# Kernel optimization log

Measured on AMD Instinct MI355X. Metric: run time of the kernel, lower is better.

## Reference

```python
import jax, jax.numpy as jnp
import numpy as np

B = 4; E_PER = 100_000; E = B * E_PER
N_NODES = 50_000; N_REL = 500; D = 64; D_LG = 256
K_PER_VI = 20; S_VI = E // K_PER_VI          # 20000 sorted vi segments
S_VJ_PER = 5_000; S_VJ = B * S_VJ_PER        # 20000 unsorted vj segments
N_MEM = 131_072
INTERACT = ((0, 3), (0, 2, 3), (0, 4), (0, 2, 4), (1, 3), (1, 2, 3), (1, 4), (1, 2, 4))


def _build_edges():
    rng = np.random.default_rng(0)
    idx_vi = np.repeat(np.arange(S_VI), K_PER_VI)          # sorted segment ids
    gpb = S_VI // B
    eg = idx_vi // gpb                                     # sorted by eg_idx too
    vi = rng.integers(0, N_NODES, S_VI)[idx_vi]
    idx_vj = np.empty(E, dtype=np.int64)
    for b in range(B):
        loc = np.concatenate([np.arange(S_VJ_PER), rng.integers(0, S_VJ_PER, E_PER - S_VJ_PER)])
        rng.shuffle(loc)
        idx_vj[b * E_PER:(b + 1) * E_PER] = b * S_VJ_PER + loc  # every group non-empty
    vj = rng.integers(0, N_NODES, S_VJ)[idx_vj]            # consistent (eg, vj) per group
    rel = rng.integers(0, N_REL, E)
    e2vi = rng.integers(0, N_MEM, E)
    e2vj = rng.integers(0, N_MEM, E)
    return np.stack([eg, vi, vj, rel, idx_vi, idx_vj, e2vi, e2vj], axis=1).astype(np.int32)


def setup_inputs() -> dict:
    key = jax.random.key(0)
    ks = jax.random.split(key, 10)
    return {
        "node_attention": jax.random.uniform(ks[0], (B, N_NODES), jnp.float32),
        "scanned_edges": jnp.asarray(_build_edges()),
        "edges_y": jax.random.uniform(ks[1], (E,), jnp.float32),
        "hidden_uncon": jax.random.normal(ks[2], (1, N_NODES, D_LG), jnp.float32),
        "hidden_con": jax.random.normal(ks[3], (N_MEM, D), jnp.float32),
        "Wc": jax.random.normal(ks[4], (D, D), jnp.float32) / np.sqrt(D).astype(np.float32),
        "bc": jnp.zeros((D,), jnp.float32),
        "Wu": jax.random.normal(ks[5], (D_LG, D), jnp.float32) / np.sqrt(D_LG).astype(np.float32),
        "bu": jnp.zeros((D,), jnp.float32),
        "rel_table": jax.random.normal(ks[6], (N_REL, D), jnp.float32) * 0.05,
        "ws": jax.random.normal(ks[7], (len(INTERACT), D), jnp.float32) / np.sqrt(float(len(INTERACT))).astype(np.float32) if False else jax.random.normal(ks[7], (len(INTERACT), D), jnp.float32) * (1.0 / np.sqrt(len(INTERACT)).astype(np.float32)),
        "fb": jnp.zeros((D,), jnp.float32),
        "out_w": jax.random.normal(ks[8], (D,), jnp.float32),
        "out_b": jnp.zeros((D,), jnp.float32),
        "n_vi_segments": S_VI,
        "n_vj_segments": S_VJ,
    }


def reference(node_attention, scanned_edges, edges_y, hidden_uncon, hidden_con,
              Wc, bc, Wu, bu, rel_table, ws, fb, out_w, out_b,
              n_vi_segments, n_vj_segments):
    eg, vi, vj, rel = (scanned_edges[:, i] for i in range(4))
    idx_vi, idx_vj, e2vi, e2vj = (scanned_edges[:, i] for i in range(4, 8))
    # projections (proj_con / proj_uncon, tanh Dense)
    hc = jnp.tanh(hidden_con @ Wc + bc)          # [N_MEM, D]
    hu = jnp.tanh(hidden_uncon @ Wu + bu)[0]     # [n_nodes, D]; batch_size==1 path of Node2Edge
    # Node2Edge gathers
    feats = (hc[e2vi], hu[vi], rel_table[rel], hc[e2vj], hu[vj])  # each [E, D]
    # F layer: weighted sum of elementwise interaction products
    out = fb
    for k, idxs in enumerate(INTERACT):
        x = feats[idxs[0]]
        for i in idxs[1:]:
            x = x * feats[i]
        out = out + x * ws[k]
    out = jax.nn.relu(out) * out_w + out_b
    logits = jnp.sum(out, axis=1)                # [E]
    # NeighborSoftmax at 'vi' (sorted segment softmax)
    m = jax.ops.segment_max(logits, idx_vi, num_segments=n_vi_segments)
    ex = jnp.exp(logits - m[idx_vi])
    den = jax.ops.segment_sum(ex, idx_vi, num_segments=n_vi_segments)
    transition = ex / den[idx_vi]
    # attention flow: gather source attention, weight, aggregate at vj
    trans_att = transition * node_attention[eg, vi] * edges_y
    aggr = jax.ops.segment_sum(trans_att, idx_vj, num_segments=n_vj_segments)
    b_g = jax.ops.segment_max(eg, idx_vj, num_segments=n_vj_segments)
    vj_g = jax.ops.segment_max(vj, idx_vj, num_segments=n_vj_segments)
    new_node_attention = jnp.zeros_like(node_attention).at[b_g, vj_g].add(aggr)
    return new_node_attention
```

## Files before the change

kernel.cpp:

```cpp
#include <hip/hip_runtime.h>
#include <hip/hip_bf16.h>
#include <hip/hip_fp16.h>

#define D 64
#define KPER 20

typedef __attribute__((ext_vector_type(8))) short short8;
typedef __attribute__((ext_vector_type(4))) float floatx4;

__device__ __forceinline__ unsigned short f2bfu(float x) {
    __hip_bfloat16 h = __float2bfloat16(x);
    return *reinterpret_cast<unsigned short*>(&h);
}
__device__ __forceinline__ unsigned short f2hu(float x) {
    __half h = __float2half(x);
    return *reinterpret_cast<unsigned short*>(&h);
}
union UH2 { unsigned u; __half2 h; };
__device__ __forceinline__ __half2 u2h2(unsigned u) { UH2 x; x.u = u; return x.h; }

__device__ __forceinline__ unsigned cvt2bf(float lo, float hi) {
    unsigned r;
    asm("v_cvt_pk_bf16_f32 %0, %1, %2" : "=v"(r) : "v"(lo), "v"(hi));
    return r;
}

__device__ __forceinline__ __half2 pk_max(__half2 a, __half2 b) {
    __half2 r;
    asm("v_pk_max_f16 %0, %1, %2" : "=v"(r) : "v"(a), "v"(b));
    return r;
}

__device__ __forceinline__ float fast_tanh(float x) {
    float xc = fminf(fmaxf(x, -15.f), 15.f);
    float e = __expf(2.f * xc);
    return 1.f - 2.f * __builtin_amdgcn_rcpf(1.f + e);
}

template<int CTRL>
__device__ __forceinline__ float dpp_add(float x) {
    int t = __builtin_amdgcn_update_dpp(0, __float_as_int(x), CTRL, 0xf, 0xf, true);
    return x + __int_as_float(t);
}
template<int CTRL>
__device__ __forceinline__ float dpp_max(float x) {
    int xi = __float_as_int(x);
    int t = __builtin_amdgcn_update_dpp(xi, xi, CTRL, 0xf, 0xf, false);
    return fmaxf(x, __int_as_float(t));
}
__device__ __forceinline__ float wave_sum_b(float x) {
    x = dpp_add<0x111>(x); x = dpp_add<0x112>(x);
    x = dpp_add<0x114>(x); x = dpp_add<0x118>(x);
    x = dpp_add<0x142>(x); x = dpp_add<0x143>(x);
    return __int_as_float(__builtin_amdgcn_readlane(__float_as_int(x), 63));
}
__device__ __forceinline__ float wave_max_b(float x) {
    x = dpp_max<0x111>(x); x = dpp_max<0x112>(x);
    x = dpp_max<0x114>(x); x = dpp_max<0x118>(x);
    x = dpp_max<0x142>(x); x = dpp_max<0x143>(x);
    return __int_as_float(__builtin_amdgcn_readlane(__float_as_int(x), 63));
}
__device__ __forceinline__ float row16_sum(float x) {
    x = dpp_add<0x111>(x); x = dpp_add<0x112>(x);
    x = dpp_add<0x114>(x); x = dpp_add<0x118>(x);
    return x;
}

__global__ __launch_bounds__(256) void prep(
        const float* __restrict__ Wc, const float* __restrict__ Wu,
        const float* __restrict__ relf, const float* __restrict__ wsf,
        const float* __restrict__ fbf,
        unsigned short* __restrict__ Wcp, unsigned short* __restrict__ Wup,
        unsigned short* __restrict__ relb, unsigned short* __restrict__ wsh,
        unsigned short* __restrict__ fbh, float* __restrict__ outz,
        int nout, int nrel) {
    int tid = blockIdx.x * 256 + threadIdx.x;
    int nth = gridDim.x * 256;
    for (int i = tid; i < 4 * 2 * 64 * 8; i += nth) {
        int j = i & 7, lane = (i >> 3) & 63, f = i >> 9;
        int ct = f >> 1, kt = f & 1;
        int m = lane & 15, quad = lane >> 4;
        Wcp[i] = f2bfu(Wc[(kt * 32 + quad * 8 + j) * 64 + ct * 16 + m]);
    }
    for (int i = tid; i < 4 * 8 * 64 * 8; i += nth) {
        int j = i & 7, lane = (i >> 3) & 63, f = i >> 9;
        int ct = f >> 3, kt = f & 7;
        int m = lane & 15, quad = lane >> 4;
        Wup[i] = f2bfu(Wu[(kt * 32 + quad * 8 + j) * 64 + ct * 16 + m]);
    }
    for (int i = tid; i < nrel; i += nth) relb[i] = f2hu(relf[i]);
    for (int i = tid; i < 8 * D; i += nth) wsh[i] = f2hu(wsf[i]);
    for (int i = tid; i < D; i += nth) fbh[i] = f2hu(fbf[i]);
    for (int i = tid; i < nout; i += nth) outz[i] = 0.0f;
}

__device__ __forceinline__ void proj64_pair(const float* __restrict__ h,
        const unsigned short* __restrict__ Wp, const float* __restrict__ b,
        unsigned short* __restrict__ out, int rt0) {
    constexpr int K = 64, KT = 2, CTN = 4;
    int lane = threadIdx.x & 63;
    int m = lane & 15, quad = lane >> 4;
    short8 bfr[CTN][KT];
    #pragma unroll
    for (int ct = 0; ct < CTN; ++ct)
        #pragma unroll
        for (int kt = 0; kt < KT; ++kt)
            bfr[ct][kt] = *(const short8*)(Wp + (((ct * 2 + kt) * 64 + lane) << 3));
    float bv[CTN];
    #pragma unroll
    for (int ct = 0; ct < CTN; ++ct) bv[ct] = b[ct * 16 + m];
    int rt1 = rt0 + 1;
    const float* hrow0 = h + (size_t)(rt0 * 16 + m) * K + quad * 8;
    const float* hrow1 = h + (size_t)(rt1 * 16 + m) * K + quad * 8;
    floatx4 a0[KT][2], a1[KT][2];
    #pragma unroll
    for (int kt = 0; kt < KT; ++kt) {
        a0[kt][0] = *(const floatx4*)(hrow0 + kt * 32);
        a0[kt][1] = *(const floatx4*)(hrow0 + kt * 32 + 4);
        a1[kt][0] = *(const floatx4*)(hrow1 + kt * 32);
        a1[kt][1] = *(const floatx4*)(hrow1 + kt * 32 + 4);
    }
    #pragma unroll
    for (int t = 0; t < 2; ++t) {
        floatx4 (*ar)[2] = t ? a1 : a0;
        int rt = t ? rt1 : rt0;
        floatx4 acc[CTN];
        #pragma unroll
        for (int ct = 0; ct < CTN; ++ct) acc[ct] = floatx4{0.f, 0.f, 0.f, 0.f};
        #pragma unroll
        for (int kt = 0; kt < KT; ++kt) {
            union { uint4 u; short8 s; } cc;
            cc.u.x = cvt2bf(ar[kt][0][0], ar[kt][0][1]);
            cc.u.y = cvt2bf(ar[kt][0][2], ar[kt][0][3]);
            cc.u.z = cvt2bf(ar[kt][1][0], ar[kt][1][1]);
            cc.u.w = cvt2bf(ar[kt][1][2], ar[kt][1][3]);
            short8 af = cc.s;
            #pragma unroll
            for (int ct = 0; ct < CTN; ++ct)
                acc[ct] = __builtin_amdgcn_mfma_f32_16x16x32_bf16(af, bfr[ct][kt], acc[ct], 0, 0, 0);
        }
        #pragma unroll
        for (int ct = 0; ct < CTN; ++ct) {
            int col = ct * 16 + m;
            #pragma unroll
            for (int reg = 0; reg < 4; ++reg) {
                int row = rt * 16 + quad * 4 + reg;
                out[(size_t)row * 64 + col] = f2hu(fast_tanh(acc[ct][reg] + bv[ct]));
            }
        }
    }
}

__device__ __forceinline__ void proj256_body(const float* __restrict__ h,
        const unsigned short* __restrict__ Wp, const float* __restrict__ b,
        unsigned short* __restrict__ out, int ct0, int rt0, int rtstride, int ntiles) {
    constexpr int K = 256, KT = 8, CTN = 2;
    int lane = threadIdx.x & 63;
    int m = lane & 15, quad = lane >> 4;
    short8 bfr[CTN][KT];
    #pragma unroll
    for (int ct = 0; ct < CTN; ++ct)
        #pragma unroll
        for (int kt = 0; kt < KT; ++kt)
            bfr[ct][kt] = *(const short8*)(Wp + ((((ct0 + ct) * 8 + kt) * 64 + lane) << 3));
    float bv[CTN];
    #pragma unroll
    for (int ct = 0; ct < CTN; ++ct) bv[ct] = b[(ct0 + ct) * 16 + m];
    for (int rt = rt0; rt < ntiles; rt += rtstride) {
        floatx4 acc[CTN];
        #pragma unroll
        for (int ct = 0; ct < CTN; ++ct) acc[ct] = floatx4{0.f, 0.f, 0.f, 0.f};
        const float* hrow = h + (size_t)(rt * 16 + m) * K + quad * 8;
        #pragma unroll
        for (int kt = 0; kt < KT; ++kt) {
            floatx4 v0 = *(const floatx4*)(hrow + kt * 32);
            floatx4 v1 = *(const floatx4*)(hrow + kt * 32 + 4);
            union { uint4 u; short8 s; } cc;
            cc.u.x = cvt2bf(v0[0], v0[1]);
            cc.u.y = cvt2bf(v0[2], v0[3]);
            cc.u.z = cvt2bf(v1[0], v1[1]);
            cc.u.w = cvt2bf(v1[2], v1[3]);
            short8 af = cc.s;
            #pragma unroll
            for (int ct = 0; ct < CTN; ++ct)
                acc[ct] = __builtin_amdgcn_mfma_f32_16x16x32_bf16(af, bfr[ct][kt], acc[ct], 0, 0, 0);
        }
        #pragma unroll
        for (int ct = 0; ct < CTN; ++ct) {
            int col = (ct0 + ct) * 16 + m;
            #pragma unroll
            for (int reg = 0; reg < 4; ++reg) {
                int row = rt * 16 + quad * 4 + reg;
                out[(size_t)row * 64 + col] = f2hu(fast_tanh(acc[ct][reg] + bv[ct]));
            }
        }
    }
}

__global__ __launch_bounds__(256) void proj_fused(
        const float* __restrict__ hcon, const unsigned short* __restrict__ Wcp,
        const float* __restrict__ bc,
        const float* __restrict__ hun, const unsigned short* __restrict__ Wup,
        const float* __restrict__ bu,
        unsigned short* __restrict__ hc, unsigned short* __restrict__ hu,
        int t64, int t256, int g64, int g256) {
    int bid = blockIdx.x;
    int w = threadIdx.x >> 6;
    if (bid < g256) {
        int wid = bid * 4 + w;
        int half = wid & 1;
        proj256_body(hun, Wup, bu, hu, half * 2, wid >> 1, g256 * 2, t256);
    } else {
        int wid = (bid - g256) * 4 + w;
        proj64_pair(hcon, Wcp, bc, hc, wid * 2);
    }
}

__device__ __forceinline__ float edge_acc(
        uint2 G0, uint2 G2, uint2 G3, uint2 G4, uint2 F1u,
        const uint2* __restrict__ wku, uint2 fbu, floatx4 owv, __half2 z2) {
    float acc = 0.f;
    #pragma unroll
    for (int p = 0; p < 2; ++p) {
        __half2 F0 = u2h2(p ? G0.y : G0.x);
        __half2 F2 = u2h2(p ? G2.y : G2.x);
        __half2 F3 = u2h2(p ? G3.y : G3.x);
        __half2 F4 = u2h2(p ? G4.y : G4.x);
        __half2 f1 = u2h2(p ? F1u.y : F1u.x);
        __half2 fb2 = u2h2(p ? fbu.y : fbu.x);
        __half2 w0 = u2h2(p ? wku[0].y : wku[0].x);
        __half2 w1 = u2h2(p ? wku[1].y : wku[1].x);
        __half2 w2 = u2h2(p ? wku[2].y : wku[2].x);
        __half2 w3 = u2h2(p ? wku[3].y : wku[3].x);
        __half2 w4 = u2h2(p ? wku[4].y : wku[4].x);
        __half2 w5 = u2h2(p ? wku[5].y : wku[5].x);
        __half2 w6 = u2h2(p ? wku[6].y : wku[6].x);
        __half2 w7 = u2h2(p ? wku[7].y : wku[7].x);
        __half2 t1 = __hfma2(F2, w1, w0);
        __half2 t2 = __hfma2(F2, w5, w4);
        __half2 t3 = __hfma2(F2, w3, w2);
        __half2 t4 = __hfma2(F2, w7, w6);
        __half2 uu = __hfma2(F0, t1, __hmul2(f1, t2));
        __half2 vv = __hfma2(F0, t3, __hmul2(f1, t4));
        __half2 od = __hfma2(F3, uu, __hfma2(F4, vv, fb2));
        __half2 r  = pk_max(od, z2);
        float2 rf  = __half22float2(r);
        acc = fmaf(rf.x, owv[2 * p], fmaf(rf.y, owv[2 * p + 1], acc));
    }
    return acc;
}

__global__ __launch_bounds__(256) void edge_kernel(
        const float* __restrict__ natt, const int* __restrict__ edges,
        const float* __restrict__ ey, const unsigned short* __restrict__ hc,
        const unsigned short* __restrict__ hu, const unsigned short* __restrict__ relt,
        const unsigned short* __restrict__ wsh, const unsigned short* __restrict__ fbh,
        const float* __restrict__ outw, float* __restrict__ out, int N) {
    int lane = threadIdx.x & 63;
    int g = lane >> 4, sub = lane & 15;
    int l2 = lane >> 2;
    int wid = blockIdx.x * 4 + (threadIdx.x >> 6);
    long baseA = (long)(wid * 2) * KPER;
    long baseB = baseA + KPER;
    const int* ebA = edges + baseA * 8;
    const int* ebB = edges + baseB * 8;

    int2 h0A = *(const int2*)ebA;
    int2 h0B = *(const int2*)ebB;
    const int* egpA = ebA + g * 8;
    const int* egpB = ebB + g * 8;
    int2 m23A[5], m67A[5], m23B[5], m67B[5];
    #pragma unroll
    for (int i = 0; i < 5; ++i) {
        m23A[i] = *(const int2*)(egpA + i * 32 + 2);
        m67A[i] = *(const int2*)(egpA + i * 32 + 6);
        m23B[i] = *(const int2*)(egpB + i * 32 + 2);
        m67B[i] = *(const int2*)(egpB + i * 32 + 6);
    }
    int myvjA = 0, myvjB = 0; float eyA = 0.f, eyB = 0.f;
    if (lane < KPER) {
        myvjA = ebA[lane * 8 + 2];
        myvjB = ebB[lane * 8 + 2];
        eyA = ey[baseA + lane];
        eyB = ey[baseB + lane];
    }
    int egA = __builtin_amdgcn_readfirstlane(h0A.x);
    int viA = __builtin_amdgcn_readfirstlane(h0A.y);
    int egB = __builtin_amdgcn_readfirstlane(h0B.x);
    int viB = __builtin_amdgcn_readfirstlane(h0B.y);
    uint2 F1A = *(const uint2*)(hu + (size_t)viA * D + sub * 4);
    uint2 F1B = *(const uint2*)(hu + (size_t)viB * D + sub * 4);
    float naA = natt[(size_t)egA * N + viA];
    float naB = natt[(size_t)egB * N + viB];

    uint2 wku[8];
    #pragma unroll
    for (int k = 0; k < 8; ++k) wku[k] = *(const uint2*)(wsh + k * D + sub * 4);
    uint2 fbu = *(const uint2*)(fbh + sub * 4);
    floatx4 owv = *(const floatx4*)(outw + sub * 4);
    __half2 z2 = __float2half2_rn(0.f);

    float mylA = -INFINITY, mylB = -INFINITY;
    uint2 c0 = *(const uint2*)(hc   + (size_t)m67A[0].x * D + sub * 4);
    uint2 c2 = *(const uint2*)(relt + (size_t)m23A[0].y * D + sub * 4);
    uint2 c3 = *(const uint2*)(hc   + (size_t)m67A[0].y * D + sub * 4);
    uint2 c4 = *(const uint2*)(hu   + (size_t)m23A[0].x * D + sub * 4);
    #pragma unroll
    for (int t = 0; t < 10; ++t) {
        uint2 n0 = c0, n2 = c2, n3 = c3, n4 = c4;
        if (t < 9) {
            const int tn = t + 1;
            const int2* p23 = (tn < 5) ? m23A : m23B;
            const int2* p67 = (tn < 5) ? m67A : m67B;
            const int ii = (tn < 5) ? tn : tn - 5;
            n0 = *(const uint2*)(hc   + (size_t)p67[ii].x * D + sub * 4);
            n2 = *(const uint2*)(relt + (size_t)p23[ii].y * D + sub * 4);
            n3 = *(const uint2*)(hc   + (size_t)p67[ii].y * D + sub * 4);
            n4 = *(const uint2*)(hu   + (size_t)p23[ii].x * D + sub * 4);
        }
        __builtin_amdgcn_sched_barrier(0);
        uint2 F1 = (t < 5) ? F1A : F1B;
        float acc = edge_acc(c0, c2, c3, c4, F1, wku, fbu, owv, z2);
        float rs = row16_sum(acc);
        float tot = __shfl(rs, ((lane & 3) << 4) + 15);
        if (t < 5) mylA = (l2 == t) ? tot : mylA;
        else       mylB = (l2 == (t - 5)) ? tot : mylB;
        c0 = n0; c2 = n2; c3 = n3; c4 = n4;
    }

    float mxA = wave_max_b(mylA);
    float exA = __expf(mylA - mxA);
    float denA = wave_sum_b(exA);
    if (lane < KPER) {
        float t = (exA / denA) * naA * eyA;
        atomicAdd(out + (size_t)egA * N + myvjA, t);
    }
    float mxB = wave_max_b(mylB);
    float exB = __expf(mylB - mxB);
    float denB = wave_sum_b(exB);
    if (lane < KPER) {
        float t = (exB / denB) * naB * eyB;
        atomicAdd(out + (size_t)egB * N + myvjB, t);
    }
}

extern "C" void kernel_launch(void* const* d_in, const int* in_sizes, int n_in,
                              void* d_out, int out_size, void* d_ws, size_t ws_size,
                              hipStream_t stream) {
    const float* natt = (const float*)d_in[0];
    const int*   edges = (const int*)d_in[1];
    const float* ey   = (const float*)d_in[2];
    const float* hun  = (const float*)d_in[3];
    const float* hcon = (const float*)d_in[4];
    const float* Wc   = (const float*)d_in[5];
    const float* bc   = (const float*)d_in[6];
    const float* Wu   = (const float*)d_in[7];
    const float* bu   = (const float*)d_in[8];
    const float* relt = (const float*)d_in[9];
    const float* wsm  = (const float*)d_in[10];
    const float* fb   = (const float*)d_in[11];
    const float* outw = (const float*)d_in[12];
    float* out = (float*)d_out;

    int E    = in_sizes[2];
    int S    = E / KPER;
    int nmem = in_sizes[4] / D;
    int N    = in_sizes[3] / 256;
    int nrel = in_sizes[9];

    int t64  = nmem / 16;
    int t256 = N / 16;
    int g64  = t64 / 8;
    int g256 = 800;

    unsigned short* hc  = (unsigned short*)d_ws;
    unsigned short* hu  = hc + (size_t)nmem * D;
    unsigned short* rb  = hu + (size_t)N * D;
    unsigned short* Wcp = rb + nrel;
    unsigned short* Wup = Wcp + 4096;
    unsigned short* wsh = Wup + 16384;
    unsigned short* fbh = wsh + 8 * D;

    prep<<<64, 256, 0, stream>>>(Wc, Wu, relt, wsm, fb, Wcp, Wup, rb, wsh, fbh,
                                 out, out_size, nrel);
    proj_fused<<<g256 + g64, 256, 0, stream>>>(hcon, Wcp, bc, hun, Wup, bu,
                                               hc, hu, t64, t256, g64, g256);
    edge_kernel<<<S / 8, 256, 0, stream>>>(natt, edges, ey, hc, hu, rb,
                                           wsh, fbh, outw, out, N);
}
```

Before: 199.3 us.

## Gather 8 edges per wave with 16-byte loads and issue all gathers upfront

Remaps the edge kernel so each wave processes 8 edges at a time with 8 lanes per edge, using 16-byte vector loads instead of 8-byte ones. All gathers for both segments are issued before any compute, replacing the one-step software prefetch pipeline. The per-edge reduction shrinks to an 8-lane DPP sum. Register pressure rises sharply, which launch_bounds(256,3) tries to cap. The 20-edge segments also waste 4 of 24 edge slots per segment.

```diff
diff --git a/kernel.cpp b/kernel.cpp
--- a/kernel.cpp
+++ b/kernel.cpp
@@ -18,6 +18,9 @@
 }
 union UH2 { unsigned u; __half2 h; };
 __device__ __forceinline__ __half2 u2h2(unsigned u) { UH2 x; x.u = u; return x.h; }
+__device__ __forceinline__ unsigned pick4(uint4 v, int p) {
+    return p == 0 ? v.x : p == 1 ? v.y : p == 2 ? v.z : v.w;
+}
 
 __device__ __forceinline__ unsigned cvt2bf(float lo, float hi) {
     unsigned r;
@@ -60,9 +63,9 @@
     x = dpp_max<0x142>(x); x = dpp_max<0x143>(x);
     return __int_as_float(__builtin_amdgcn_readlane(__float_as_int(x), 63));
 }
-__device__ __forceinline__ float row16_sum(float x) {
+__device__ __forceinline__ float row8_sum(float x) {
     x = dpp_add<0x111>(x); x = dpp_add<0x112>(x);
-    x = dpp_add<0x114>(x); x = dpp_add<0x118>(x);
+    x = dpp_add<0x114>(x);
     return x;
 }
 
@@ -216,26 +219,27 @@
     }
 }
 
-__device__ __forceinline__ float edge_acc(
-        uint2 G0, uint2 G2, uint2 G3, uint2 G4, uint2 F1u,
-        const uint2* __restrict__ wku, uint2 fbu, floatx4 owv, __half2 z2) {
+__device__ __forceinline__ float edge_acc8(
+        uint4 G0, uint4 G2, uint4 G3, uint4 G4, uint4 F1,
+        const uint4* __restrict__ wk4, uint4 fb4,
+        floatx4 ow0, floatx4 ow1, __half2 z2) {
     float acc = 0.f;
     #pragma unroll
-    for (int p = 0; p < 2; ++p) {
-        __half2 F0 = u2h2(p ? G0.y : G0.x);
-        __half2 F2 = u2h2(p ? G2.y : G2.x);
-        __half2 F3 = u2h2(p ? G3.y : G3.x);
-        __half2 F4 = u2h2(p ? G4.y : G4.x);
-        __half2 f1 = u2h2(p ? F1u.y : F1u.x);
-        __half2 fb2 = u2h2(p ? fbu.y : fbu.x);
-        __half2 w0 = u2h2(p ? wku[0].y : wku[0].x);
-        __half2 w1 = u2h2(p ? wku[1].y : wku[1].x);
-        __half2 w2 = u2h2(p ? wku[2].y : wku[2].x);
-        __half2 w3 = u2h2(p ? wku[3].y : wku[3].x);
-        __half2 w4 = u2h2(p ? wku[4].y : wku[4].x);
-        __half2 w5 = u2h2(p ? wku[5].y : wku[5].x);
-        __half2 w6 = u2h2(p ? wku[6].y : wku[6].x);
-        __half2 w7 = u2h2(p ? wku[7].y : wku[7].x);
+    for (int p = 0; p < 4; ++p) {
+        __half2 F0 = u2h2(pick4(G0, p));
+        __half2 F2 = u2h2(pick4(G2, p));
+        __half2 F3 = u2h2(pick4(G3, p));
+        __half2 F4 = u2h2(pick4(G4, p));
+        __half2 f1 = u2h2(pick4(F1, p));
+        __half2 fb2 = u2h2(pick4(fb4, p));
+        __half2 w0 = u2h2(pick4(wk4[0], p));
+        __half2 w1 = u2h2(pick4(wk4[1], p));
+        __half2 w2 = u2h2(pick4(wk4[2], p));
+        __half2 w3 = u2h2(pick4(wk4[3], p));
+        __half2 w4 = u2h2(pick4(wk4[4], p));
+        __half2 w5 = u2h2(pick4(wk4[5], p));
+        __half2 w6 = u2h2(pick4(wk4[6], p));
+        __half2 w7 = u2h2(pick4(wk4[7], p));
         __half2 t1 = __hfma2(F2, w1, w0);
         __half2 t2 = __hfma2(F2, w5, w4);
         __half2 t3 = __hfma2(F2, w3, w2);
@@ -245,20 +249,21 @@
         __half2 od = __hfma2(F3, uu, __hfma2(F4, vv, fb2));
         __half2 r  = pk_max(od, z2);
         float2 rf  = __half22float2(r);
-        acc = fmaf(rf.x, owv[2 * p], fmaf(rf.y, owv[2 * p + 1], acc));
+        float owa = (p < 2) ? ow0[2 * p]     : ow1[2 * p - 4];
+        float owb = (p < 2) ? ow0[2 * p + 1] : ow1[2 * p - 3];
+        acc = fmaf(rf.x, owa, fmaf(rf.y, owb, acc));
     }
     return acc;
 }
 
-__global__ __launch_bounds__(256) void edge_kernel(
+__global__ __launch_bounds__(256, 3) void edge_kernel(
         const float* __restrict__ natt, const int* __restrict__ edges,
         const float* __restrict__ ey, const unsigned short* __restrict__ hc,
         const unsigned short* __restrict__ hu, const unsigned short* __restrict__ relt,
         const unsigned short* __restrict__ wsh, const unsigned short* __restrict__ fbh,
         const float* __restrict__ outw, float* __restrict__ out, int N) {
     int lane = threadIdx.x & 63;
-    int g = lane >> 4, sub = lane & 15;
-    int l2 = lane >> 2;
+    int g8 = lane >> 3, sub8 = lane & 7;
     int wid = blockIdx.x * 4 + (threadIdx.x >> 6);
     long baseA = (long)(wid * 2) * KPER;
     long baseB = baseA + KPER;
@@ -267,15 +272,14 @@
 
     int2 h0A = *(const int2*)ebA;
     int2 h0B = *(const int2*)ebB;
-    const int* egpA = ebA + g * 8;
-    const int* egpB = ebB + g * 8;
-    int2 m23A[5], m67A[5], m23B[5], m67B[5];
-    #pragma unroll
-    for (int i = 0; i < 5; ++i) {
-        m23A[i] = *(const int2*)(egpA + i * 32 + 2);
-        m67A[i] = *(const int2*)(egpA + i * 32 + 6);
-        m23B[i] = *(const int2*)(egpB + i * 32 + 2);
-        m67B[i] = *(const int2*)(egpB + i * 32 + 6);
+    int2 m23A[3], m67A[3], m23B[3], m67B[3];
+    #pragma unroll
+    for (int t = 0; t < 3; ++t) {
+        int e = t * 8 + g8; e = (e < KPER) ? e : (KPER - 1);
+        m23A[t] = *(const int2*)(ebA + e * 8 + 2);
+        m67A[t] = *(const int2*)(ebA + e * 8 + 6);
+        m23B[t] = *(const int2*)(ebB + e * 8 + 2);
+        m67B[t] = *(const int2*)(ebB + e * 8 + 6);
     }
     int myvjA = 0, myvjB = 0; float eyA = 0.f, eyB = 0.f;
     if (lane < KPER) {
@@ -288,59 +292,64 @@
     int viA = __builtin_amdgcn_readfirstlane(h0A.y);
     int egB = __builtin_amdgcn_readfirstlane(h0B.x);
     int viB = __builtin_amdgcn_readfirstlane(h0B.y);
-    uint2 F1A = *(const uint2*)(hu + (size_t)viA * D + sub * 4);
-    uint2 F1B = *(const uint2*)(hu + (size_t)viB * D + sub * 4);
+
+    uint4 GA0[3], GA2[3], GA3[3], GA4[3];
+    #pragma unroll
+    for (int t = 0; t < 3; ++t) {
+        GA0[t] = *(const uint4*)(hc   + (size_t)m67A[t].x * D + sub8 * 8);
+        GA2[t] = *(const uint4*)(relt + (size_t)m23A[t].y * D + sub8 * 8);
+        GA3[t] = *(const uint4*)(hc   + (size_t)m67A[t].y * D + sub8 * 8);
+        GA4[t] = *(const uint4*)(hu   + (size_t)m23A[t].x * D + sub8 * 8);
+    }
+    uint4 F1A = *(const uint4*)(hu + (size_t)viA * D + sub8 * 8);
+    uint4 GB0[3], GB2[3], GB3[3], GB4[3];
+    #pragma unroll
+    for (int t = 0; t < 3; ++t) {
+        GB0[t] = *(const uint4*)(hc   + (size_t)m67B[t].x * D + sub8 * 8);
+        GB2[t] = *(const uint4*)(relt + (size_t)m23B[t].y * D + sub8 * 8);
+        GB3[t] = *(const uint4*)(hc   + (size_t)m67B[t].y * D + sub8 * 8);
+        GB4[t] = *(const uint4*)(hu   + (size_t)m23B[t].x * D + sub8 * 8);
+    }
+    uint4 F1B = *(const uint4*)(hu + (size_t)viB * D + sub8 * 8);
     float naA = natt[(size_t)egA * N + viA];
     float naB = natt[(size_t)egB * N + viB];
 
-    uint2 wku[8];
-    #pragma unroll
-    for (int k = 0; k < 8; ++k) wku[k] = *(const uint2*)(wsh + k * D + sub * 4);
-    uint2 fbu = *(const uint2*)(fbh + sub * 4);
-    floatx4 owv = *(const floatx4*)(outw + sub * 4);
+    uint4 wk4[8];
+    #pragma unroll
+    for (int k = 0; k < 8; ++k) wk4[k] = *(const uint4*)(wsh + k * D + sub8 * 8);
+    uint4 fb4 = *(const uint4*)(fbh + sub8 * 8);
+    floatx4 ow0 = *(const floatx4*)(outw + sub8 * 8);
+    floatx4 ow1 = *(const floatx4*)(outw + sub8 * 8 + 4);
     __half2 z2 = __float2half2_rn(0.f);
 
     float mylA = -INFINITY, mylB = -INFINITY;
-    uint2 c0 = *(const uint2*)(hc   + (size_t)m67A[0].x * D + sub * 4);
-    uint2 c2 = *(const uint2*)(relt + (size_t)m23A[0].y * D + sub * 4);
-    uint2 c3 = *(const uint2*)(hc   + (size_t)m67A[0].y * D + sub * 4);
-    uint2 c4 = *(const uint2*)(hu   + (size_t)m23A[0].x * D + sub * 4);
-    #pragma unroll
-    for (int t = 0; t < 10; ++t) {
-        uint2 n0 = c0, n2 = c2, n3 = c3, n4 = c4;
-        if (t < 9) {
-            const int tn = t + 1;
-            const int2* p23 = (tn < 5) ? m23A : m23B;
-            const int2* p67 = (tn < 5) ? m67A : m67B;
-            const int ii = (tn < 5) ? tn : tn - 5;
-            n0 = *(const uint2*)(hc   + (size_t)p67[ii].x * D + sub * 4);
-            n2 = *(const uint2*)(relt + (size_t)p23[ii].y * D + sub * 4);
-            n3 = *(const uint2*)(hc   + (size_t)p67[ii].y * D + sub * 4);
-            n4 = *(const uint2*)(hu   + (size_t)p23[ii].x * D + sub * 4);
-        }
-        __builtin_amdgcn_sched_barrier(0);
-        uint2 F1 = (t < 5) ? F1A : F1B;
-        float acc = edge_acc(c0, c2, c3, c4, F1, wku, fbu, owv, z2);
-        float rs = row16_sum(acc);
-        float tot = __shfl(rs, ((lane & 3) << 4) + 15);
-        if (t < 5) mylA = (l2 == t) ? tot : mylA;
-        else       mylB = (l2 == (t - 5)) ? tot : mylB;
-        c0 = n0; c2 = n2; c3 = n3; c4 = n4;
-    }
-
+    #pragma unroll
+    for (int t = 0; t < 3; ++t) {
+        float acc = edge_acc8(GA0[t], GA2[t], GA3[t], GA4[t], F1A, wk4, fb4, ow0, ow1, z2);
+        float rs = row8_sum(acc);
+        float tot = __shfl(rs, ((lane & 7) << 3) + 7);
+        mylA = ((lane >> 3) == t && lane < KPER) ? tot : mylA;
+    }
     float mxA = wave_max_b(mylA);
     float exA = __expf(mylA - mxA);
     float denA = wave_sum_b(exA);
     if (lane < KPER) {
-        float t = (exA / denA) * naA * eyA;
-        atomicAdd(out + (size_t)egA * N + myvjA, t);
+        float tv = (exA / denA) * naA * eyA;
+        atomicAdd(out + (size_t)egA * N + myvjA, tv);
+    }
+    #pragma unroll
+    for (int t = 0; t < 3; ++t) {
+        float acc = edge_acc8(GB0[t], GB2[t], GB3[t], GB4[t], F1B, wk4, fb4, ow0, ow1, z2);
+        float rs = row8_sum(acc);
+        float tot = __shfl(rs, ((lane & 7) << 3) + 7);
+        mylB = ((lane >> 3) == t && lane < KPER) ? tot : mylB;
     }
     float mxB = wave_max_b(mylB);
     float exB = __expf(mylB - mxB);
     float denB = wave_sum_b(exB);
     if (lane < KPER) {
-        float t = (exB / denB) * naB * eyB;
-        atomicAdd(out + (size_t)egB * N + myvjB, t);
+        float tv = (exB / denB) * naB * eyB;
+        atomicAdd(out + (size_t)egB * N + myvjB, tv);
     }
 }
 
```

Measured after the change: 193.0 us. 1.03x faster.
